# Optimization experiments

Measured on AMD Instinct MI355X. Metric: run time of the kernel, lower is better.

The kernel has to match this reference:

```python
import jax, jax.numpy as jnp
import numpy as np

B, C, H, W = 8, 128, 64, 64


def setup_inputs() -> dict:
    key = jax.random.key(0)
    ks = jax.random.split(key, 7)
    query_img = jax.random.normal(ks[0], (B, C, H, W), dtype=jnp.float32)
    key_img = jax.random.normal(ks[1], (B, C, H, W), dtype=jnp.float32)
    value_img = jax.random.normal(ks[2], (B, C, H, W), dtype=jnp.float32)
    # 1x1 conv weights == dense [out, in] matrices (kaiming-ish scale)
    scale = 1.0 / np.sqrt(C)
    Wq = jax.random.normal(ks[3], (C, C), dtype=jnp.float32) * scale
    bq = jax.random.normal(ks[4], (C,), dtype=jnp.float32) * scale
    Wk = jax.random.normal(ks[5], (C, C), dtype=jnp.float32) * scale
    bk = jax.random.normal(ks[6], (C,), dtype=jnp.float32) * scale
    return {"query_img": query_img, "key_img": key_img, "value_img": value_img,
            "Wq": Wq, "bq": bq, "Wk": Wk, "bk": bk}


def reference(query_img, key_img, value_img, Wq, bq, Wk, bk):
    b, c, h, w = query_img.shape
    hw = h * w
    # 1x1 convs as GEMMs -> token-major layout (b, hw, c_out)
    q = jnp.einsum('bchw,oc->bhwo', query_img, Wq).reshape(b, hw, -1) + bq
    k = jnp.einsum('bchw,oc->bohw', key_img, Wk).reshape(b, -1, hw) + bk[None, :, None]
    # scores scaled by sqrt(HW) (faithful: key.size(-1) == h*w in source)
    scores = jnp.einsum('bqc,bck->bqk', q, k) / jnp.sqrt(jnp.float32(hw))
    attn = jax.nn.softmax(scores, axis=-1)  # (b, hw, hw)
    v = value_img.reshape(b, c, hw).transpose(0, 2, 1)  # (b, hw, c)
    out = jnp.einsum('bqk,bkc->bqc', attn, v)  # (b, hw, c)
    out = out.transpose(0, 2, 1).reshape(b, -1, h, w)
    out = out + q.transpose(0, 2, 1).reshape(b, -1, h, w)  # residual from query proj
    return out
```

## Files before the change

### kernel.cpp

```cpp
#include <hip/hip_runtime.h>

#define BB 8
#define CC 128
#define SS 4096
#define KT 64
#define NSPLIT 2
#define HKV (SS / NSPLIT)
#define NIT (HKV / KT)
#define SCALE 0.015625f

typedef __attribute__((ext_vector_type(8))) short sh8;
typedef __attribute__((ext_vector_type(4))) float f32x4;

__device__ __forceinline__ float b2f(unsigned short u) {
    union { unsigned int i; float f; } x; x.i = ((unsigned int)u) << 16; return x.f;
}
__device__ __forceinline__ unsigned short f2b(float f) {
    union { float f; unsigned int i; } x; x.f = f;
    unsigned int r = x.i + 0x7fff + ((x.i >> 16) & 1);
    return (unsigned short)(r >> 16);
}
__device__ __forceinline__ unsigned short rhu(float f) {
    union { float f; unsigned int i; } x; x.f = f;
    return (unsigned short)((x.i + 0x8000) >> 16);
}
__device__ __forceinline__ unsigned int cvtpk(float lo, float hi) {
    unsigned int r;
    asm("v_cvt_pk_bf16_f32 %0, %1, %2" : "=v"(r) : "v"(lo), "v"(hi));
    return r;
}

__device__ __forceinline__ void dma16(const void* g, void* l) {
    __builtin_amdgcn_global_load_lds((const __attribute__((address_space(1))) void*)g,
                                     (__attribute__((address_space(3))) void*)l,
                                     16, 0, 0);
}

__global__ __launch_bounds__(256) void cvt_kernel(
    const float* __restrict__ vimg,
    const float* __restrict__ Wq, const float* __restrict__ Wk,
    const float* __restrict__ bq, const float* __restrict__ bk,
    unsigned short* __restrict__ Vbuf,
    unsigned short* __restrict__ Wqb, unsigned short* __restrict__ Wkb,
    unsigned short* __restrict__ bqb, unsigned short* __restrict__ bkb)
{
    const int bx = blockIdx.x, tid = threadIdx.x;
    if (bx < 512) {
        const size_t base = (size_t)bx * 8192 + tid * 4;
        #pragma unroll
        for (int it = 0; it < 8; ++it) {
            const size_t i = base + (size_t)it * 1024;
            float4 v = *(const float4*)(vimg + i);
            ushort4 o;
            o.x = f2b(v.x); o.y = f2b(v.y); o.z = f2b(v.z); o.w = f2b(v.w);
            *(ushort4*)(Vbuf + i) = o;
        }
    } else {
        const int w = bx - 512;
        for (int e = w * 256 + tid; e < 33024; e += 2048) {
            float v; unsigned short* dst;
            if (e < 16384)      { v = Wq[e];         dst = Wqb + e; }
            else if (e < 32768) { v = Wk[e - 16384]; dst = Wkb + (e - 16384); }
            else if (e < 32896) { v = bq[e - 32768]; dst = bqb + (e - 32768); }
            else                { v = bk[e - 32896]; dst = bkb + (e - 32896); }
            *dst = f2b(v);
        }
    }
}

__global__ __launch_bounds__(256) void proj_kernel(
    const float* __restrict__ qimg, const float* __restrict__ kimg,
    const unsigned short* __restrict__ Wqb, const unsigned short* __restrict__ Wkb,
    const unsigned short* __restrict__ bqb, const unsigned short* __restrict__ bkb,
    unsigned short* __restrict__ Qbuf, unsigned short* __restrict__ Kbuf)
{
    __shared__ float ilds[128 * 69];

    const int z = blockIdx.z;
    const float* img = (z == 0) ? qimg : kimg;
    const unsigned short* Wb = (z == 0) ? Wqb : Wkb;
    const unsigned short* bias = (z == 0) ? bqb : bkb;
    unsigned short* outTok = (z == 0) ? Qbuf : Kbuf;

    const int tid  = threadIdx.x;
    const int wave = tid >> 6;
    const int lane = tid & 63;
    const int l15  = lane & 15;
    const int quad = lane >> 4;
    const int b     = blockIdx.y;
    const int stile = blockIdx.x;

    const float* gbase = img + (size_t)b * CC * SS + stile * 64;
    #pragma unroll
    for (int i = 0; i < 8; ++i) {
        const int l = tid + 256 * i;
        const int row = l >> 4, col = (l & 15) * 4;
        float4 v = *(const float4*)(gbase + (size_t)row * SS + col);
        float* d = ilds + row * 69 + col;
        d[0] = v.x; d[1] = v.y; d[2] = v.z; d[3] = v.w;
    }
    __syncthreads();

    const int tcol = wave * 16 + l15;
    sh8 a[4];
    #pragma unroll
    for (int kk = 0; kk < 4; ++kk)
        #pragma unroll
        for (int j = 0; j < 8; ++j)
            a[kk][j] = (short)rhu(ilds[(32 * kk + quad * 8 + j) * 69 + tcol]);

    f32x4 acc[8];
    #pragma unroll
    for (int nt = 0; nt < 8; ++nt) acc[nt] = (f32x4){0.f, 0.f, 0.f, 0.f};

    #pragma unroll
    for (int nt = 0; nt < 8; ++nt) {
        const unsigned short* wp = Wb + (size_t)(16 * nt + l15) * CC + quad * 8;
        #pragma unroll
        for (int kk = 0; kk < 4; ++kk) {
            sh8 bf = *(const sh8*)(wp + 32 * kk);
            acc[nt] = __builtin_amdgcn_mfma_f32_16x16x32_bf16(a[kk], bf, acc[nt], 0, 0, 0);
        }
    }

    __syncthreads();
    unsigned short* oT = (unsigned short*)ilds;
    #pragma unroll
    for (int nt = 0; nt < 8; ++nt) {
        const int o = 16 * nt + l15;
        const float bv = b2f(bias[o]);
        #pragma unroll
        for (int r = 0; r < 4; ++r) {
            const int sl = wave * 16 + quad * 4 + r;
            oT[sl * 132 + o] = f2b(acc[nt][r] + bv);
        }
    }
    __syncthreads();

    unsigned short* orow = outTok + ((size_t)b * SS + stile * 64) * CC;
    #pragma unroll
    for (int i = 0; i < 8; ++i) {
        const int idx = tid + 256 * i;
        const int s = idx >> 5, o4 = (idx & 31) * 4;
        *(ushort4*)(orow + (size_t)s * CC + o4) = *(const ushort4*)(oT + s * 132 + o4);
    }
}

__global__ __launch_bounds__(256, 2) void attn_kernel(
    const unsigned short* __restrict__ Qbuf,
    const unsigned short* __restrict__ Kbuf,
    const unsigned short* __restrict__ Vbuf,
    float* __restrict__ Oout,
    float* __restrict__ Lsum)
{
    __shared__ __align__(16) unsigned char smem[65536];

    const int tid  = threadIdx.x;
    const int wave = tid >> 6;
    const int lane = tid & 63;
    const int l15  = lane & 15;
    const int quad = lane >> 4;
    const int wgid = blockIdx.x;
    const int b    = wgid & 7;
    const int half = (wgid >> 3) & 1;
    const int qt   = wgid >> 4;
    const int qbase = qt * 128 + wave * 32;
    const int tok0  = half * HKV;

    const unsigned short* kbp = Kbuf + (size_t)b * SS * CC;
    const unsigned short* vbp = Vbuf + (size_t)b * CC * SS;

    sh8 aq[2][4];
    #pragma unroll
    for (int m = 0; m < 2; ++m) {
        const unsigned short* qp = Qbuf + ((size_t)b * SS + qbase + m * 16 + l15) * CC + quad * 8;
        #pragma unroll
        for (int kk = 0; kk < 4; ++kk) aq[m][kk] = *(const sh8*)(qp + 32 * kk);
    }

    int kGO[4], vGO[4];
    #pragma unroll
    for (int j = 0; j < 4; ++j) {
        const int krow = wave * 16 + j * 4 + quad;
        const int sx = (krow & 3) | ((krow >> 1) & 4);
        kGO[j] = krow * 256 + (((lane & 15) ^ sx) << 4);
        const int vrow = (wave * 4 + j) * 8 + (lane >> 3);
        vGO[j] = vrow * 8192 + (((lane & 7) ^ ((lane >> 3) & 7)) << 4);
    }

    int krb[4];
    #pragma unroll
    for (int n = 0; n < 4; ++n)
        krb[n] = (32 * (n >> 1) + 8 * (l15 >> 2) + 4 * (n & 1) + (l15 & 3)) * 256;
    const int krs = l15 & 7;

    f32x4 oacc[2][8];
    #pragma unroll
    for (int m = 0; m < 2; ++m)
        #pragma unroll
        for (int ct = 0; ct < 8; ++ct) oacc[m][ct] = (f32x4){0.f, 0.f, 0.f, 0.f};
    float lsum[2] = {0.f, 0.f};

    const char* gk0 = (const char*)kbp + (size_t)tok0 * 256;
    const char* gv0 = (const char*)vbp + (size_t)tok0 * 2;

    #pragma unroll
    for (int j = 0; j < 4; ++j) {
        dma16(gk0 + kGO[j], smem + (wave * 4 + j) * 1024);
        dma16(gv0 + vGO[j], smem + 32768 + (wave * 4 + j) * 1024);
    }

    for (int it = 0; it < NIT; ++it) {
        unsigned char* kb = smem + ((it & 1) << 14);
        unsigned char* vb = smem + 32768 + ((it & 1) << 14);

        __syncthreads();

        if (it + 1 < NIT) {
            const char* gk = gk0 + (size_t)(it + 1) * KT * 256;
            const char* gv = gv0 + (size_t)(it + 1) * KT * 2;
            unsigned char* kbn = smem + (((it + 1) & 1) << 14);
            unsigned char* vbn = smem + 32768 + (((it + 1) & 1) << 14);
            #pragma unroll
            for (int j = 0; j < 4; ++j) {
                dma16(gk + kGO[j], kbn + (wave * 4 + j) * 1024);
                dma16(gv + vGO[j], vbn + (wave * 4 + j) * 1024);
            }
        }

        f32x4 sacc[2][4];
        #pragma unroll
        for (int m = 0; m < 2; ++m)
            #pragma unroll
            for (int n = 0; n < 4; ++n) sacc[m][n] = (f32x4){0.f, 0.f, 0.f, 0.f};
        __builtin_amdgcn_s_setprio(1);
        #pragma unroll
        for (int n = 0; n < 4; ++n) {
            #pragma unroll
            for (int kk = 0; kk < 4; ++kk) {
                sh8 kf = *(const sh8*)(kb + krb[n] + (((4 * kk + quad) ^ krs) << 4));
                sacc[0][n] = __builtin_amdgcn_mfma_f32_16x16x32_bf16(kf, aq[0][kk], sacc[0][n], 0, 0, 0);
                sacc[1][n] = __builtin_amdgcn_mfma_f32_16x16x32_bf16(kf, aq[1][kk], sacc[1][n], 0, 0, 0);
            }
        }
        __builtin_amdgcn_s_setprio(0);

        union { sh8 v; unsigned int d[4]; } pa[2][2];
        #pragma unroll
        for (int m = 0; m < 2; ++m) {
            float p[4][4];
            #pragma unroll
            for (int n = 0; n < 4; ++n)
                #pragma unroll
                for (int r = 0; r < 4; ++r) {
                    p[n][r] = __expf(sacc[m][n][r] * SCALE);
                    lsum[m] += p[n][r];
                }
            #pragma unroll
            for (int kp = 0; kp < 2; ++kp) {
                pa[m][kp].d[0] = cvtpk(p[2 * kp][0],     p[2 * kp][1]);
                pa[m][kp].d[1] = cvtpk(p[2 * kp][2],     p[2 * kp][3]);
                pa[m][kp].d[2] = cvtpk(p[2 * kp + 1][0], p[2 * kp + 1][1]);
                pa[m][kp].d[3] = cvtpk(p[2 * kp + 1][2], p[2 * kp + 1][3]);
            }
        }

        __builtin_amdgcn_s_setprio(1);
        #pragma unroll
        for (int kp = 0; kp < 2; ++kp) {
            #pragma unroll
            for (int ct = 0; ct < 8; ++ct) {
                sh8 bv = *(const sh8*)(vb + (16 * ct + l15) * 128
                                          + (((kp * 4 + quad) ^ (l15 & 7)) << 4));
                oacc[0][ct] = __builtin_amdgcn_mfma_f32_16x16x32_bf16(pa[0][kp].v, bv, oacc[0][ct], 0, 0, 0);
                oacc[1][ct] = __builtin_amdgcn_mfma_f32_16x16x32_bf16(pa[1][kp].v, bv, oacc[1][ct], 0, 0, 0);
            }
        }
        __builtin_amdgcn_s_setprio(0);
    }

    #pragma unroll
    for (int m = 0; m < 2; ++m) {
        lsum[m] += __shfl_xor(lsum[m], 16, 64);
        lsum[m] += __shfl_xor(lsum[m], 32, 64);
    }
    if (quad == 0) {
        float* lp = Lsum + ((size_t)half * BB + b) * SS + qbase;
        lp[l15]      = lsum[0];
        lp[16 + l15] = lsum[1];
    }

    __syncthreads();

    unsigned short* oT = (unsigned short*)smem;
    #pragma unroll
    for (int m = 0; m < 2; ++m)
        #pragma unroll
        for (int ct = 0; ct < 8; ++ct) {
            const int c  = 16 * ct + l15;
            const int q0 = wave * 32 + m * 16 + quad * 4;
            ushort4 o;
            o.x = rhu(oacc[m][ct][0]); o.y = rhu(oacc[m][ct][1]);
            o.z = rhu(oacc[m][ct][2]); o.w = rhu(oacc[m][ct][3]);
            *(ushort4*)(oT + c * 136 + q0) = o;
        }
    __syncthreads();

    char* ob = (char*)Oout;
    #pragma unroll
    for (int i = 0; i < 16; ++i) {
        const int idx = tid + 256 * i;
        const int c = idx >> 5, q4 = (idx & 31) * 4;
        const size_t rb = ((size_t)(b * CC + c) * SS + (size_t)qt * 128) * 4;
        *(ushort4*)(ob + rb + half * 256 + q4 * 2) = *(const ushort4*)(oT + c * 136 + q4);
    }
}

__global__ __launch_bounds__(256) void combine_kernel(
    const unsigned short* __restrict__ Qbuf,
    const float* __restrict__ Lsum,
    float* __restrict__ out)
{
    const int b = blockIdx.y, qt = blockIdx.x, tid = threadIdx.x;
    const int s0l  = (tid & 31) * 4;
    const int coff = tid >> 5;

    const int s0 = qt * 128 + s0l;
    float4 l0 = *(const float4*)(Lsum + (size_t)b * SS + s0);
    float4 l1 = *(const float4*)(Lsum + ((size_t)BB + b) * SS + s0);
    float rinv[4];
    rinv[0] = 1.f / (l0.x + l1.x); rinv[1] = 1.f / (l0.y + l1.y);
    rinv[2] = 1.f / (l0.z + l1.z); rinv[3] = 1.f / (l0.w + l1.w);

    const unsigned short* qb = Qbuf + ((size_t)b * SS + s0) * CC;

    for (int k = 0; k < 16; ++k) {
        const int c = coff + 8 * k;
        const size_t rb = (size_t)(b * CC + c) * SS + (size_t)qt * 128;
        ushort4 p0 = *(const ushort4*)((const char*)out + rb * 4 + s0l * 2);
        ushort4 p1 = *(const ushort4*)((const char*)out + rb * 4 + 256 + s0l * 2);
        const float r0 = b2f(qb[(size_t)0 * CC + c]);
        const float r1 = b2f(qb[(size_t)1 * CC + c]);
        const float r2 = b2f(qb[(size_t)2 * CC + c]);
        const float r3 = b2f(qb[(size_t)3 * CC + c]);
        __syncthreads();
        float4 o;
        o.x = (b2f(p0.x) + b2f(p1.x)) * rinv[0] + r0;
        o.y = (b2f(p0.y) + b2f(p1.y)) * rinv[1] + r1;
        o.z = (b2f(p0.z) + b2f(p1.z)) * rinv[2] + r2;
        o.w = (b2f(p0.w) + b2f(p1.w)) * rinv[3] + r3;
        *(float4*)(out + rb + s0l) = o;
    }
}

extern "C" void kernel_launch(void* const* d_in, const int* in_sizes, int n_in,
                              void* d_out, int out_size, void* d_ws, size_t ws_size,
                              hipStream_t stream) {
    const float* qimg = (const float*)d_in[0];
    const float* kimg = (const float*)d_in[1];
    const float* vimg = (const float*)d_in[2];
    const float* Wq   = (const float*)d_in[3];
    const float* bq   = (const float*)d_in[4];
    const float* Wk   = (const float*)d_in[5];
    const float* bk   = (const float*)d_in[6];
    float* out = (float*)d_out;

    unsigned short* Qbuf = (unsigned short*)d_ws;
    unsigned short* Kbuf = Qbuf + (size_t)BB * SS * CC;
    unsigned short* Vbuf = Kbuf + (size_t)BB * SS * CC;
    unsigned short* Wqb  = Vbuf + (size_t)BB * SS * CC;
    unsigned short* Wkb  = Wqb + CC * CC;
    unsigned short* bqb  = Wkb + CC * CC;
    unsigned short* bkb  = bqb + CC;
    float* Lsum = (float*)(bkb + CC);

    cvt_kernel<<<dim3(520), 256, 0, stream>>>(vimg, Wq, Wk, bq, bk,
                                              Vbuf, Wqb, Wkb, bqb, bkb);
    proj_kernel<<<dim3(SS / 64, BB, 2), 256, 0, stream>>>(
        qimg, kimg, Wqb, Wkb, bqb, bkb, Qbuf, Kbuf);
    attn_kernel<<<dim3(NSPLIT * BB * (SS / 128)), 256, 0, stream>>>(
        Qbuf, Kbuf, Vbuf, out, Lsum);
    combine_kernel<<<dim3(SS / 128, BB), 256, 0, stream>>>(Qbuf, Lsum, out);
}
```

Measured before the change: 196.4 us.

## Fuse split-KV combine into attention kernel via last-arriver atomic flag

```diff
diff --git a/kernel.cpp b/kernel.cpp
--- a/kernel.cpp
+++ b/kernel.cpp
@@ -42,7 +42,8 @@
     const float* __restrict__ bq, const float* __restrict__ bk,
     unsigned short* __restrict__ Vbuf,
     unsigned short* __restrict__ Wqb, unsigned short* __restrict__ Wkb,
-    unsigned short* __restrict__ bqb, unsigned short* __restrict__ bkb)
+    unsigned short* __restrict__ bqb, unsigned short* __restrict__ bkb,
+    int* __restrict__ flags)
 {
     const int bx = blockIdx.x, tid = threadIdx.x;
     if (bx < 512) {
@@ -56,6 +57,7 @@
             *(ushort4*)(Vbuf + i) = o;
         }
     } else {
+        if (bx == 512) flags[tid] = 0;
         const int w = bx - 512;
         for (int e = w * 256 + tid; e < 33024; e += 2048) {
             float v; unsigned short* dst;
@@ -151,7 +153,8 @@
     const unsigned short* __restrict__ Kbuf,
     const unsigned short* __restrict__ Vbuf,
     float* __restrict__ Oout,
-    float* __restrict__ Lsum)
+    float* __restrict__ Lsum,
+    int* __restrict__ flags)
 {
     __shared__ __align__(16) unsigned char smem[65536];
 
@@ -314,42 +317,46 @@
         const size_t rb = ((size_t)(b * CC + c) * SS + (size_t)qt * 128) * 4;
         *(ushort4*)(ob + rb + half * 256 + q4 * 2) = *(const ushort4*)(oT + c * 136 + q4);
     }
-}
-
-__global__ __launch_bounds__(256) void combine_kernel(
-    const unsigned short* __restrict__ Qbuf,
-    const float* __restrict__ Lsum,
-    float* __restrict__ out)
-{
-    const int b = blockIdx.y, qt = blockIdx.x, tid = threadIdx.x;
-    const int s0l  = (tid & 31) * 4;
-    const int coff = tid >> 5;
-
-    const int s0 = qt * 128 + s0l;
-    float4 l0 = *(const float4*)(Lsum + (size_t)b * SS + s0);
-    float4 l1 = *(const float4*)(Lsum + ((size_t)BB + b) * SS + s0);
+
+    __threadfence();
+    __syncthreads();
+    if (tid == 0)
+        *(volatile int*)smem = atomicAdd(&flags[b * 32 + qt], 1);
+    __syncthreads();
+    const int old = *(volatile int*)smem;
+    if (old == 0) return;
+
+    __threadfence();
+
+    unsigned short (*rS)[133] = (unsigned short(*)[133])smem;
+    const unsigned short* qb2 = Qbuf + ((size_t)b * SS + qt * 128) * CC;
+    #pragma unroll
+    for (int i = 0; i < 16; ++i) {
+        const int idx = tid + 256 * i;
+        const int s = idx >> 5, c4 = (idx & 31) * 4;
+        *(ushort4*)(&rS[s][c4]) = *(const ushort4*)(qb2 + (size_t)s * CC + c4);
+    }
+
+    const int s0l = (tid & 31) * 4;
+    float4 l0 = *(const float4*)(Lsum + (size_t)b * SS + qt * 128 + s0l);
+    float4 l1 = *(const float4*)(Lsum + ((size_t)BB + b) * SS + qt * 128 + s0l);
     float rinv[4];
     rinv[0] = 1.f / (l0.x + l1.x); rinv[1] = 1.f / (l0.y + l1.y);
     rinv[2] = 1.f / (l0.z + l1.z); rinv[3] = 1.f / (l0.w + l1.w);
-
-    const unsigned short* qb = Qbuf + ((size_t)b * SS + s0) * CC;
-
+    __syncthreads();
+
+    const int coff = tid >> 5;
     for (int k = 0; k < 16; ++k) {
         const int c = coff + 8 * k;
         const size_t rb = (size_t)(b * CC + c) * SS + (size_t)qt * 128;
-        ushort4 p0 = *(const ushort4*)((const char*)out + rb * 4 + s0l * 2);
-        ushort4 p1 = *(const ushort4*)((const char*)out + rb * 4 + 256 + s0l * 2);
-        const float r0 = b2f(qb[(size_t)0 * CC + c]);
-        const float r1 = b2f(qb[(size_t)1 * CC + c]);
-        const float r2 = b2f(qb[(size_t)2 * CC + c]);
-        const float r3 = b2f(qb[(size_t)3 * CC + c]);
-        __syncthreads();
+        ushort4 p0 = *(const ushort4*)((const char*)Oout + rb * 4 + s0l * 2);
+        ushort4 p1 = *(const ushort4*)((const char*)Oout + rb * 4 + 256 + s0l * 2);
         float4 o;
-        o.x = (b2f(p0.x) + b2f(p1.x)) * rinv[0] + r0;
-        o.y = (b2f(p0.y) + b2f(p1.y)) * rinv[1] + r1;
-        o.z = (b2f(p0.z) + b2f(p1.z)) * rinv[2] + r2;
-        o.w = (b2f(p0.w) + b2f(p1.w)) * rinv[3] + r3;
-        *(float4*)(out + rb + s0l) = o;
+        o.x = (b2f(p0.x) + b2f(p1.x)) * rinv[0] + b2f(rS[s0l + 0][c]);
+        o.y = (b2f(p0.y) + b2f(p1.y)) * rinv[1] + b2f(rS[s0l + 1][c]);
+        o.z = (b2f(p0.z) + b2f(p1.z)) * rinv[2] + b2f(rS[s0l + 2][c]);
+        o.w = (b2f(p0.w) + b2f(p1.w)) * rinv[3] + b2f(rS[s0l + 3][c]);
+        *(float4*)(Oout + rb + s0l) = o;
     }
 }
 
@@ -373,12 +380,12 @@
     unsigned short* bqb  = Wkb + CC * CC;
     unsigned short* bkb  = bqb + CC;
     float* Lsum = (float*)(bkb + CC);
+    int* flags  = (int*)(Lsum + (size_t)NSPLIT * BB * SS);
 
     cvt_kernel<<<dim3(520), 256, 0, stream>>>(vimg, Wq, Wk, bq, bk,
-                                              Vbuf, Wqb, Wkb, bqb, bkb);
+                                              Vbuf, Wqb, Wkb, bqb, bkb, flags);
     proj_kernel<<<dim3(SS / 64, BB, 2), 256, 0, stream>>>(
         qimg, kimg, Wqb, Wkb, bqb, bkb, Qbuf, Kbuf);
     attn_kernel<<<dim3(NSPLIT * BB * (SS / 128)), 256, 0, stream>>>(
-        Qbuf, Kbuf, Vbuf, out, Lsum);
-    combine_kernel<<<dim3(SS / 128, BB), 256, 0, stream>>>(Qbuf, Lsum, out);
-}
+        Qbuf, Kbuf, Vbuf, out, Lsum, flags);
+}
```

After: 264.1 us. +34.5%, slower.
